# Kernel optimization log

Measured on AMD Instinct MI355X. Metric: run time of the kernel, lower is better.

The kernel has to match this reference:

```python
import jax, jax.numpy as jnp
import numpy as np

B, C, D = 1024, 1000, 256
EPS = 1e-4


def setup_inputs() -> dict:
    key = jax.random.key(0)
    k_z, k_mu = jax.random.split(key)
    z = jax.random.normal(k_z, (B, D), dtype=jnp.float32)
    mu = jax.random.normal(k_mu, (C, D), dtype=jnp.float32)  # init.normal_(mu, 0, 1)
    prior_logits = jnp.zeros((C,), dtype=jnp.float32)          # init.zeros_
    precision_factor = jnp.eye(D, dtype=jnp.float32)           # init.eye_
    return {"z": z, "mu": mu, "prior_logits": prior_logits,
            "precision_factor": precision_factor}


def reference(z, mu, prior_logits, precision_factor):
    # Shared precision matrix: symmetrized F F^T + eps I  -> (D, D)
    precision = precision_factor @ precision_factor.T
    precision = 0.5 * (precision + precision.T)
    precision = precision + EPS * jnp.eye(D, dtype=precision_factor.dtype)

    log_prior = jax.nn.log_softmax(prior_logits)  # (C,)

    # Mahalanobis distance per (sample, class): (z-mu)^T P (z-mu)
    diff = z[:, None, :] - mu[None, :, :]                      # (B, C, D)
    m2 = jnp.einsum('bcd,de,bce->bc', diff, precision, diff)   # (B, C)

    return log_prior[None, :] - 0.5 * m2
```

## Files before the change

kernel.cpp:

```cpp
#include <hip/hip_runtime.h>
#include <hip/hip_bf16.h>
#include <math.h>

constexpr int Bn = 1024;
constexpr int Cn = 1000;
constexpr int Dn = 256;
constexpr float EPS = 1e-4f;

typedef __attribute__((ext_vector_type(8))) short bf16x8;
typedef __attribute__((ext_vector_type(4))) float f32x4;

static __device__ __forceinline__ unsigned short f2bf(float x) {
    union { float f; unsigned u; } v; v.f = x;
    unsigned r = (v.u + 0x7fffu + ((v.u >> 16) & 1u)) >> 16;
    return (unsigned short)r;
}

__global__ __launch_bounds__(256) void prep_kernel(const float* __restrict__ z,
                                                   const float* __restrict__ mu,
                                                   const float* __restrict__ logits,
                                                   const float* __restrict__ F,
                                                   unsigned short* __restrict__ Yb,
                                                   unsigned short* __restrict__ Ub,
                                                   float* __restrict__ rn_part,
                                                   float* __restrict__ cn_part,
                                                   float* __restrict__ epsn_z,
                                                   float* __restrict__ epsn_mu,
                                                   float* __restrict__ lse_out) {
    __shared__ float As[64][68];
    __shared__ float Bs[64][36];
    __shared__ float red[64][17];
    const int bid = blockIdx.x, tid = threadIdx.x;

    if (bid == 256) {
        float* rl = &red[0][0];
        float mx = -INFINITY;
        for (int i = tid; i < Cn; i += 256) mx = fmaxf(mx, logits[i]);
        rl[tid] = mx; __syncthreads();
        for (int s = 128; s > 0; s >>= 1) {
            if (tid < s) rl[tid] = fmaxf(rl[tid], rl[tid + s]);
            __syncthreads();
        }
        mx = rl[0]; __syncthreads();
        float sm = 0.f;
        for (int i = tid; i < Cn; i += 256) sm += expf(logits[i] - mx);
        rl[tid] = sm; __syncthreads();
        for (int s = 128; s > 0; s >>= 1) {
            if (tid < s) rl[tid] += rl[tid + s];
            __syncthreads();
        }
        if (tid == 0) *lse_out = mx + logf(rl[0]);
        return;
    }

    const bool isMu = bid >= 128;
    const int  b    = isMu ? bid - 128 : bid;
    const float* X  = isMu ? mu : z;
    unsigned short* XB = isMu ? Ub : Yb;
    float* npart    = isMu ? cn_part : rn_part;
    float* epsn     = isMu ? epsn_mu : epsn_z;
    const int M     = isMu ? Cn : Bn;
    const int row0  = (b >> 3) * 64;
    const int ct    = b & 7;
    const int col0  = ct * 32;
    const int tx = tid & 15, ty = tid >> 4;

    float acc[4][2] = {};

    for (int kt = 0; kt < Dn; kt += 64) {
#pragma unroll
        for (int it = 0; it < 4; ++it) {
            const int l  = tid + it * 256;
            const int r  = l >> 4;
            const int kc = (l & 15) << 2;
            int gr = row0 + r;
            if (gr > M - 1) gr = M - 1;
            const float4 va = *(const float4*)&X[(size_t)gr * Dn + kt + kc];
            As[kc + 0][r] = va.x; As[kc + 1][r] = va.y;
            As[kc + 2][r] = va.z; As[kc + 3][r] = va.w;
        }
#pragma unroll
        for (int it = 0; it < 2; ++it) {
            const int l  = tid + it * 256;
            const int r  = l >> 3;
            const int kc = (l & 7) << 2;
            *(float4*)&Bs[r][kc] = *(const float4*)&F[(size_t)(kt + r) * Dn + col0 + kc];
        }
        __syncthreads();
#pragma unroll
        for (int k = 0; k < 64; ++k) {
            const float4 a  = *(const float4*)&As[k][ty << 2];
            const float2 bb = *(const float2*)&Bs[k][tx << 1];
            acc[0][0] = fmaf(a.x, bb.x, acc[0][0]);
            acc[0][1] = fmaf(a.x, bb.y, acc[0][1]);
            acc[1][0] = fmaf(a.y, bb.x, acc[1][0]);
            acc[1][1] = fmaf(a.y, bb.y, acc[1][1]);
            acc[2][0] = fmaf(a.z, bb.x, acc[2][0]);
            acc[2][1] = fmaf(a.z, bb.y, acc[2][1]);
            acc[3][0] = fmaf(a.w, bb.x, acc[3][0]);
            acc[3][1] = fmaf(a.w, bb.y, acc[3][1]);
        }
        __syncthreads();
    }

#pragma unroll
    for (int i = 0; i < 4; ++i) {
        const int gr = row0 + (ty << 2) + i;
        ushort2 s;
        s.x = f2bf(acc[i][0]);
        s.y = f2bf(acc[i][1]);
        *(ushort2*)&XB[(size_t)gr * Dn + col0 + (tx << 1)] = s;
    }

#pragma unroll
    for (int i = 0; i < 4; ++i)
        red[(ty << 2) + i][tx] = acc[i][0] * acc[i][0] + acc[i][1] * acc[i][1];
    __syncthreads();
    if (tid < 64) {
        float s = 0.f;
#pragma unroll
        for (int x = 0; x < 16; ++x) s += red[tid][x];
        npart[(size_t)(row0 + tid) * 8 + ct] = s;
    }

    if (ct == 0) {
        const int r = tid >> 2, q = tid & 3;
        int gr = row0 + r;
        if (gr > M - 1) gr = M - 1;
        const float4* px = (const float4*)&X[(size_t)gr * Dn + (q << 6)];
        float s = 0.f;
#pragma unroll
        for (int i = 0; i < 16; ++i) {
            const float4 v = px[i];
            s += v.x * v.x + v.y * v.y + v.z * v.z + v.w * v.w;
        }
        __syncthreads();
        red[r][q] = s;
        __syncthreads();
        if (tid < 64)
            epsn[row0 + tid] = (row0 + tid < M)
                ? EPS * (red[tid][0] + red[tid][1] + red[tid][2] + red[tid][3])
                : 0.f;
    }
}

__global__ __launch_bounds__(256) void main_kernel(const unsigned short* __restrict__ Yb,
                                                   const unsigned short* __restrict__ Ub,
                                                   const float* __restrict__ rn_part,
                                                   const float* __restrict__ cn_part,
                                                   const float* __restrict__ epsn_z,
                                                   const float* __restrict__ epsn_mu,
                                                   const float* __restrict__ logits,
                                                   const float* __restrict__ lse_p,
                                                   float* __restrict__ out) {
    __shared__ float rowbias[64], colbias[64];
    const int tid  = threadIdx.x;
    const int col0 = blockIdx.x * 64;
    const int row0 = blockIdx.y * 64;

    if (tid < 64) {
        const int r = row0 + tid;
        const float4 p0 = *(const float4*)&rn_part[(size_t)r * 8];
        const float4 p1 = *(const float4*)&rn_part[(size_t)r * 8 + 4];
        rowbias[tid] = -0.5f * (p0.x + p0.y + p0.z + p0.w +
                                p1.x + p1.y + p1.z + p1.w + epsn_z[r]);
    } else if (tid < 128) {
        const int c = col0 + tid - 64;
        float v = 0.f;
        if (c < Cn) {
            const float4 p0 = *(const float4*)&cn_part[(size_t)c * 8];
            const float4 p1 = *(const float4*)&cn_part[(size_t)c * 8 + 4];
            v = logits[c] - *lse_p - 0.5f * (p0.x + p0.y + p0.z + p0.w +
                                             p1.x + p1.y + p1.z + p1.w + epsn_mu[c]);
        }
        colbias[tid - 64] = v;
    }

    const int lane = tid & 63, w = tid >> 6;
    const int wr = (w >> 1) * 32, wc = (w & 1) * 32;
    const int la = lane & 15, kg = lane >> 4;

    const bf16x8* pa = (const bf16x8*)&Yb[(size_t)(row0 + wr + la) * Dn + kg * 8];
    const bf16x8* pb = (const bf16x8*)&Ub[(size_t)(col0 + wc + la) * Dn + kg * 8];

    f32x4 acc00 = {0.f, 0.f, 0.f, 0.f};
    f32x4 acc01 = {0.f, 0.f, 0.f, 0.f};
    f32x4 acc10 = {0.f, 0.f, 0.f, 0.f};
    f32x4 acc11 = {0.f, 0.f, 0.f, 0.f};

#pragma unroll
    for (int kt = 0; kt < 8; ++kt) {
        const bf16x8 a0 = pa[kt * 4];
        const bf16x8 a1 = pa[kt * 4 + 512];
        const bf16x8 b0 = pb[kt * 4];
        const bf16x8 b1 = pb[kt * 4 + 512];
        acc00 = __builtin_amdgcn_mfma_f32_16x16x32_bf16(a0, b0, acc00, 0, 0, 0);
        acc01 = __builtin_amdgcn_mfma_f32_16x16x32_bf16(a0, b1, acc01, 0, 0, 0);
        acc10 = __builtin_amdgcn_mfma_f32_16x16x32_bf16(a1, b0, acc10, 0, 0, 0);
        acc11 = __builtin_amdgcn_mfma_f32_16x16x32_bf16(a1, b1, acc11, 0, 0, 0);
    }
    __syncthreads();

    const int rbase = kg * 4;
#define EPI(ACC, RF, CF)                                                      \
    do {                                                                      \
        const int gcl = wc + (CF)*16 + la;                                    \
        const int gc  = col0 + gcl;                                           \
        if (gc < Cn) {                                                        \
            const float cb = colbias[gcl];                                    \
            _Pragma("unroll")                                                 \
            for (int j = 0; j < 4; ++j) {                                     \
                const int rl = wr + (RF)*16 + rbase + j;                      \
                out[(size_t)(row0 + rl) * Cn + gc] = ACC[j] + rowbias[rl] + cb; \
            }                                                                 \
        }                                                                     \
    } while (0)

    EPI(acc00, 0, 0); EPI(acc01, 0, 1); EPI(acc10, 1, 0); EPI(acc11, 1, 1);
#undef EPI
}

extern "C" void kernel_launch(void* const* d_in, const int* in_sizes, int n_in,
                              void* d_out, int out_size, void* d_ws, size_t ws_size,
                              hipStream_t stream) {
    const float* z      = (const float*)d_in[0];
    const float* mu     = (const float*)d_in[1];
    const float* logits = (const float*)d_in[2];
    const float* F      = (const float*)d_in[3];
    float* out = (float*)d_out;

    char* ws = (char*)d_ws;
    unsigned short* Yb = (unsigned short*)(ws);
    unsigned short* Ub = (unsigned short*)(ws + (512 << 10));
    float* rn_part = (float*)(ws + (1 << 20));
    float* cn_part = (float*)(ws + (1 << 20) + (32 << 10));
    float* epsn_z  = (float*)(ws + (1 << 20) + (64 << 10));
    float* epsn_mu = epsn_z + 1024;
    float* lse     = epsn_mu + 1024;

    prep_kernel<<<dim3(257), dim3(256), 0, stream>>>(z, mu, logits, F, Yb, Ub,
                                                     rn_part, cn_part,
                                                     epsn_z, epsn_mu, lse);
    main_kernel<<<dim3(16, 16), dim3(256), 0, stream>>>(Yb, Ub, rn_part, cn_part,
                                                        epsn_z, epsn_mu, logits, lse, out);
}
```

Before: 22.60 us.

## Fuse prep and main into one cooperative kernel with MFMA projection

Merges the two launches into a single cooperative kernel with three phases separated by grid-wide syncs. Phase one converts z and mu to bf16, transposes F to bf16, and computes the eps norms and the log-sum-exp. Phase two computes the projection with bf16 MFMA instead of an fp32 FMA tile loop. Phase three derives the row and column norms from the bf16 projections and runs the final GEMM. This removes one launch and the slow fp32 prep GEMM, at the cost of two grid syncs, an extra conversion pass, and norms computed from bf16-rounded values.

```diff
diff --git a/kernel.cpp b/kernel.cpp
--- a/kernel.cpp
+++ b/kernel.cpp
@@ -1,6 +1,9 @@
 #include <hip/hip_runtime.h>
 #include <hip/hip_bf16.h>
+#include <hip/hip_cooperative_groups.h>
 #include <math.h>
+
+namespace cg = cooperative_groups;
 
 constexpr int Bn = 1024;
 constexpr int Cn = 1000;
@@ -12,28 +15,70 @@
 
 static __device__ __forceinline__ unsigned short f2bf(float x) {
     union { float f; unsigned u; } v; v.f = x;
-    unsigned r = (v.u + 0x7fffu + ((v.u >> 16) & 1u)) >> 16;
-    return (unsigned short)r;
-}
-
-__global__ __launch_bounds__(256) void prep_kernel(const float* __restrict__ z,
-                                                   const float* __restrict__ mu,
-                                                   const float* __restrict__ logits,
-                                                   const float* __restrict__ F,
-                                                   unsigned short* __restrict__ Yb,
-                                                   unsigned short* __restrict__ Ub,
-                                                   float* __restrict__ rn_part,
-                                                   float* __restrict__ cn_part,
-                                                   float* __restrict__ epsn_z,
-                                                   float* __restrict__ epsn_mu,
-                                                   float* __restrict__ lse_out) {
-    __shared__ float As[64][68];
-    __shared__ float Bs[64][36];
-    __shared__ float red[64][17];
+    return (unsigned short)((v.u + 0x7fffu + ((v.u >> 16) & 1u)) >> 16);
+}
+static __device__ __forceinline__ float bf2f(unsigned short h) {
+    union { unsigned u; float f; } v; v.u = ((unsigned)h) << 16; return v.f;
+}
+
+__global__ __launch_bounds__(256) void lda_fused_kernel(
+        const float* __restrict__ z, const float* __restrict__ mu,
+        const float* __restrict__ logits, const float* __restrict__ F,
+        unsigned short* __restrict__ Gb,
+        unsigned short* __restrict__ Ftb,
+        unsigned short* __restrict__ Wb,
+        float* __restrict__ epsn,
+        float* __restrict__ lse_p,
+        float* __restrict__ out) {
     const int bid = blockIdx.x, tid = threadIdx.x;
-
-    if (bid == 256) {
-        float* rl = &red[0][0];
+    __shared__ float red[64][4];
+    __shared__ float rowbias[64], colbias[64];
+    __shared__ float rl[256];
+
+    if (bid < 16) {
+        const size_t b4 = (size_t)bid * 4096;
+#pragma unroll
+        for (int i = 0; i < 16; ++i) {
+            const size_t e4 = b4 + i * 256 + tid;
+            const float4 v = ((const float4*)z)[e4];
+            ushort4 s;
+            s.x = f2bf(v.x); s.y = f2bf(v.y); s.z = f2bf(v.z); s.w = f2bf(v.w);
+            ((ushort4*)Gb)[e4] = s;
+        }
+    } else if (bid < 32) {
+        const int rb = bid - 16;
+        const int r = tid >> 2, q = tid & 3;
+        const int gr = rb * 64 + r;
+        const int rm = gr < Cn ? gr : Cn - 1;
+        const float4* src = (const float4*)&mu[(size_t)rm * Dn + q * 64];
+        ushort4* dst = (ushort4*)&Gb[(size_t)(1024 + gr) * Dn + q * 64];
+#pragma unroll
+        for (int i = 0; i < 16; ++i) {
+            const float4 v = src[i];
+            ushort4 s;
+            s.x = f2bf(v.x); s.y = f2bf(v.y); s.z = f2bf(v.z); s.w = f2bf(v.w);
+            dst[i] = s;
+        }
+    } else if (bid < 64) {
+        const int eb = bid - 32;
+        const int r = tid >> 2, q = tid & 3;
+        const int g = eb * 64 + r;
+        const float* src = (g < 1024)
+            ? &z[(size_t)g * Dn]
+            : &mu[(size_t)((g - 1024) < Cn ? (g - 1024) : Cn - 1) * Dn];
+        const float4* p4 = (const float4*)&src[q * 64];
+        float s = 0.f;
+#pragma unroll
+        for (int i = 0; i < 16; ++i) {
+            const float4 v = p4[i];
+            s += v.x * v.x + v.y * v.y + v.z * v.z + v.w * v.w;
+        }
+        red[r][q] = s;
+        __syncthreads();
+        if (tid < 64)
+            epsn[eb * 64 + tid] = EPS * (red[tid][0] + red[tid][1] +
+                                         red[tid][2] + red[tid][3]);
+    } else if (bid == 64) {
         float mx = -INFINITY;
         for (int i = tid; i < Cn; i += 256) mx = fmaxf(mx, logits[i]);
         rl[tid] = mx; __syncthreads();
@@ -49,139 +94,102 @@
             if (tid < s) rl[tid] += rl[tid + s];
             __syncthreads();
         }
-        if (tid == 0) *lse_out = mx + logf(rl[0]);
-        return;
-    }
-
-    const bool isMu = bid >= 128;
-    const int  b    = isMu ? bid - 128 : bid;
-    const float* X  = isMu ? mu : z;
-    unsigned short* XB = isMu ? Ub : Yb;
-    float* npart    = isMu ? cn_part : rn_part;
-    float* epsn     = isMu ? epsn_mu : epsn_z;
-    const int M     = isMu ? Cn : Bn;
-    const int row0  = (b >> 3) * 64;
-    const int ct    = b & 7;
-    const int col0  = ct * 32;
-    const int tx = tid & 15, ty = tid >> 4;
-
-    float acc[4][2] = {};
-
-    for (int kt = 0; kt < Dn; kt += 64) {
-#pragma unroll
-        for (int it = 0; it < 4; ++it) {
-            const int l  = tid + it * 256;
-            const int r  = l >> 4;
-            const int kc = (l & 15) << 2;
-            int gr = row0 + r;
-            if (gr > M - 1) gr = M - 1;
-            const float4 va = *(const float4*)&X[(size_t)gr * Dn + kt + kc];
-            As[kc + 0][r] = va.x; As[kc + 1][r] = va.y;
-            As[kc + 2][r] = va.z; As[kc + 3][r] = va.w;
-        }
-#pragma unroll
-        for (int it = 0; it < 2; ++it) {
-            const int l  = tid + it * 256;
-            const int r  = l >> 3;
-            const int kc = (l & 7) << 2;
-            *(float4*)&Bs[r][kc] = *(const float4*)&F[(size_t)(kt + r) * Dn + col0 + kc];
-        }
-        __syncthreads();
-#pragma unroll
-        for (int k = 0; k < 64; ++k) {
-            const float4 a  = *(const float4*)&As[k][ty << 2];
-            const float2 bb = *(const float2*)&Bs[k][tx << 1];
-            acc[0][0] = fmaf(a.x, bb.x, acc[0][0]);
-            acc[0][1] = fmaf(a.x, bb.y, acc[0][1]);
-            acc[1][0] = fmaf(a.y, bb.x, acc[1][0]);
-            acc[1][1] = fmaf(a.y, bb.y, acc[1][1]);
-            acc[2][0] = fmaf(a.z, bb.x, acc[2][0]);
-            acc[2][1] = fmaf(a.z, bb.y, acc[2][1]);
-            acc[3][0] = fmaf(a.w, bb.x, acc[3][0]);
-            acc[3][1] = fmaf(a.w, bb.y, acc[3][1]);
-        }
-        __syncthreads();
-    }
-
-#pragma unroll
-    for (int i = 0; i < 4; ++i) {
-        const int gr = row0 + (ty << 2) + i;
-        ushort2 s;
-        s.x = f2bf(acc[i][0]);
-        s.y = f2bf(acc[i][1]);
-        *(ushort2*)&XB[(size_t)gr * Dn + col0 + (tx << 1)] = s;
-    }
-
-#pragma unroll
-    for (int i = 0; i < 4; ++i)
-        red[(ty << 2) + i][tx] = acc[i][0] * acc[i][0] + acc[i][1] * acc[i][1];
+        if (tid == 0) *lse_p = mx + logf(rl[0]);
+    } else if (bid >= 240) {
+        const int fb = bid - 240;
+#pragma unroll
+        for (int i = 0; i < 16; ++i) {
+            const int c = fb * 16 + i;
+            Ftb[(size_t)c * Dn + tid] = f2bf(F[(size_t)tid * Dn + c]);
+        }
+    }
+
+    cg::this_grid().sync();
+
+    {
+        const int row0 = (bid >> 3) * 64;
+        const int col0 = (bid & 7) * 32;
+        const int lane = tid & 63, w = tid >> 6;
+        const int wr = (w >> 1) * 32, wc = (w & 1) * 16;
+        const int la = lane & 15, kg = lane >> 4;
+
+        const bf16x8* pa = (const bf16x8*)&Gb[(size_t)(row0 + wr + la) * Dn + kg * 8];
+        const bf16x8* pb = (const bf16x8*)&Ftb[(size_t)(col0 + wc + la) * Dn + kg * 8];
+
+        f32x4 acc0 = {0.f, 0.f, 0.f, 0.f};
+        f32x4 acc1 = {0.f, 0.f, 0.f, 0.f};
+#pragma unroll
+        for (int kt = 0; kt < 8; ++kt) {
+            const bf16x8 b0 = pb[kt * 4];
+            const bf16x8 a0 = pa[kt * 4];
+            const bf16x8 a1 = pa[kt * 4 + 512];
+            acc0 = __builtin_amdgcn_mfma_f32_16x16x32_bf16(a0, b0, acc0, 0, 0, 0);
+            acc1 = __builtin_amdgcn_mfma_f32_16x16x32_bf16(a1, b0, acc1, 0, 0, 0);
+        }
+        const int col = col0 + wc + la;
+        const int rb0 = row0 + wr + kg * 4;
+#pragma unroll
+        for (int j = 0; j < 4; ++j) {
+            Wb[(size_t)(rb0 + j) * Dn + col]      = f2bf(acc0[j]);
+            Wb[(size_t)(rb0 + 16 + j) * Dn + col] = f2bf(acc1[j]);
+        }
+    }
+
+    cg::this_grid().sync();
+
+    const int row0 = (bid >> 4) * 64;
+    const int col0 = (bid & 15) * 64;
+    const int r = tid >> 2, q = tid & 3;
+
+    {
+        const bf16x8* py = (const bf16x8*)&Wb[(size_t)(row0 + r) * Dn + q * 64];
+        float s = 0.f;
+#pragma unroll
+        for (int i = 0; i < 8; ++i) {
+            const bf16x8 h = py[i];
+#pragma unroll
+            for (int j = 0; j < 8; ++j) {
+                const float f = bf2f((unsigned short)h[j]);
+                s = fmaf(f, f, s);
+            }
+        }
+        red[r][q] = s;
+    }
+    __syncthreads();
+    if (tid < 64)
+        rowbias[tid] = -0.5f * (red[tid][0] + red[tid][1] + red[tid][2] +
+                                red[tid][3] + epsn[row0 + tid]);
+    __syncthreads();
+    {
+        const bf16x8* pu = (const bf16x8*)&Wb[(size_t)(1024 + col0 + r) * Dn + q * 64];
+        float s = 0.f;
+#pragma unroll
+        for (int i = 0; i < 8; ++i) {
+            const bf16x8 h = pu[i];
+#pragma unroll
+            for (int j = 0; j < 8; ++j) {
+                const float f = bf2f((unsigned short)h[j]);
+                s = fmaf(f, f, s);
+            }
+        }
+        red[r][q] = s;
+    }
     __syncthreads();
     if (tid < 64) {
-        float s = 0.f;
-#pragma unroll
-        for (int x = 0; x < 16; ++x) s += red[tid][x];
-        npart[(size_t)(row0 + tid) * 8 + ct] = s;
-    }
-
-    if (ct == 0) {
-        const int r = tid >> 2, q = tid & 3;
-        int gr = row0 + r;
-        if (gr > M - 1) gr = M - 1;
-        const float4* px = (const float4*)&X[(size_t)gr * Dn + (q << 6)];
-        float s = 0.f;
-#pragma unroll
-        for (int i = 0; i < 16; ++i) {
-            const float4 v = px[i];
-            s += v.x * v.x + v.y * v.y + v.z * v.z + v.w * v.w;
-        }
-        __syncthreads();
-        red[r][q] = s;
-        __syncthreads();
-        if (tid < 64)
-            epsn[row0 + tid] = (row0 + tid < M)
-                ? EPS * (red[tid][0] + red[tid][1] + red[tid][2] + red[tid][3])
-                : 0.f;
-    }
-}
-
-__global__ __launch_bounds__(256) void main_kernel(const unsigned short* __restrict__ Yb,
-                                                   const unsigned short* __restrict__ Ub,
-                                                   const float* __restrict__ rn_part,
-                                                   const float* __restrict__ cn_part,
-                                                   const float* __restrict__ epsn_z,
-                                                   const float* __restrict__ epsn_mu,
-                                                   const float* __restrict__ logits,
-                                                   const float* __restrict__ lse_p,
-                                                   float* __restrict__ out) {
-    __shared__ float rowbias[64], colbias[64];
-    const int tid  = threadIdx.x;
-    const int col0 = blockIdx.x * 64;
-    const int row0 = blockIdx.y * 64;
-
-    if (tid < 64) {
-        const int r = row0 + tid;
-        const float4 p0 = *(const float4*)&rn_part[(size_t)r * 8];
-        const float4 p1 = *(const float4*)&rn_part[(size_t)r * 8 + 4];
-        rowbias[tid] = -0.5f * (p0.x + p0.y + p0.z + p0.w +
-                                p1.x + p1.y + p1.z + p1.w + epsn_z[r]);
-    } else if (tid < 128) {
-        const int c = col0 + tid - 64;
-        float v = 0.f;
-        if (c < Cn) {
-            const float4 p0 = *(const float4*)&cn_part[(size_t)c * 8];
-            const float4 p1 = *(const float4*)&cn_part[(size_t)c * 8 + 4];
-            v = logits[c] - *lse_p - 0.5f * (p0.x + p0.y + p0.z + p0.w +
-                                             p1.x + p1.y + p1.z + p1.w + epsn_mu[c]);
-        }
-        colbias[tid - 64] = v;
-    }
+        const int c = col0 + tid;
+        colbias[tid] = (c < Cn)
+            ? logits[c] - *lse_p - 0.5f * (red[tid][0] + red[tid][1] + red[tid][2] +
+                                           red[tid][3] + epsn[1024 + c])
+            : 0.f;
+    }
+    __syncthreads();
 
     const int lane = tid & 63, w = tid >> 6;
     const int wr = (w >> 1) * 32, wc = (w & 1) * 32;
     const int la = lane & 15, kg = lane >> 4;
 
-    const bf16x8* pa = (const bf16x8*)&Yb[(size_t)(row0 + wr + la) * Dn + kg * 8];
-    const bf16x8* pb = (const bf16x8*)&Ub[(size_t)(col0 + wc + la) * Dn + kg * 8];
+    const bf16x8* pa = (const bf16x8*)&Wb[(size_t)(row0 + wr + la) * Dn + kg * 8];
+    const bf16x8* pb = (const bf16x8*)&Wb[(size_t)(1024 + col0 + wc + la) * Dn + kg * 8];
 
     f32x4 acc00 = {0.f, 0.f, 0.f, 0.f};
     f32x4 acc01 = {0.f, 0.f, 0.f, 0.f};
@@ -199,21 +207,20 @@
         acc10 = __builtin_amdgcn_mfma_f32_16x16x32_bf16(a1, b0, acc10, 0, 0, 0);
         acc11 = __builtin_amdgcn_mfma_f32_16x16x32_bf16(a1, b1, acc11, 0, 0, 0);
     }
-    __syncthreads();
 
     const int rbase = kg * 4;
-#define EPI(ACC, RF, CF)                                                      \
-    do {                                                                      \
-        const int gcl = wc + (CF)*16 + la;                                    \
-        const int gc  = col0 + gcl;                                           \
-        if (gc < Cn) {                                                        \
-            const float cb = colbias[gcl];                                    \
-            _Pragma("unroll")                                                 \
-            for (int j = 0; j < 4; ++j) {                                     \
-                const int rl = wr + (RF)*16 + rbase + j;                      \
-                out[(size_t)(row0 + rl) * Cn + gc] = ACC[j] + rowbias[rl] + cb; \
-            }                                                                 \
-        }                                                                     \
+#define EPI(ACC, RF, CF)                                                        \
+    do {                                                                        \
+        const int gcl = wc + (CF)*16 + la;                                      \
+        const int gc  = col0 + gcl;                                             \
+        if (gc < Cn) {                                                          \
+            const float cb = colbias[gcl];                                      \
+            _Pragma("unroll")                                                   \
+            for (int j = 0; j < 4; ++j) {                                       \
+                const int rlc = wr + (RF)*16 + rbase + j;                       \
+                out[(size_t)(row0 + rlc) * Cn + gc] = ACC[j] + rowbias[rlc] + cb; \
+            }                                                                   \
+        }                                                                       \
     } while (0)
 
     EPI(acc00, 0, 0); EPI(acc01, 0, 1); EPI(acc10, 1, 0); EPI(acc11, 1, 1);
@@ -230,17 +237,15 @@
     float* out = (float*)d_out;
 
     char* ws = (char*)d_ws;
-    unsigned short* Yb = (unsigned short*)(ws);
-    unsigned short* Ub = (unsigned short*)(ws + (512 << 10));
-    float* rn_part = (float*)(ws + (1 << 20));
-    float* cn_part = (float*)(ws + (1 << 20) + (32 << 10));
-    float* epsn_z  = (float*)(ws + (1 << 20) + (64 << 10));
-    float* epsn_mu = epsn_z + 1024;
-    float* lse     = epsn_mu + 1024;
-
-    prep_kernel<<<dim3(257), dim3(256), 0, stream>>>(z, mu, logits, F, Yb, Ub,
-                                                     rn_part, cn_part,
-                                                     epsn_z, epsn_mu, lse);
-    main_kernel<<<dim3(16, 16), dim3(256), 0, stream>>>(Yb, Ub, rn_part, cn_part,
-                                                        epsn_z, epsn_mu, logits, lse, out);
-}
+    unsigned short* Wb  = (unsigned short*)(ws);
+    unsigned short* Gb  = (unsigned short*)(ws + (1 << 20));
+    unsigned short* Ftb = (unsigned short*)(ws + (2 << 20));
+    float* epsn = (float*)(ws + (2 << 20) + (128 << 10));
+    float* lse  = epsn + 2048;
+
+    void* args[] = { (void*)&z, (void*)&mu, (void*)&logits, (void*)&F,
+                     (void*)&Gb, (void*)&Ftb, (void*)&Wb,
+                     (void*)&epsn, (void*)&lse, (void*)&out };
+    hipLaunchCooperativeKernel((const void*)lda_fused_kernel,
+                               dim3(256), dim3(256), args, 0, stream);
+}
```

Result: slower. 86.53 us (+282.9%).
